# Performance work log

Hardware: AMD Instinct MI355X
Metric: run time of the kernel (lower is better)

The kernel has to match this reference:

```python
import jax, jax.numpy as jnp
import numpy as np

TOP_K = 8
NUM_EXPERTS = 256
HIDDEN = 7168
NUM_TOKENS = 16384
NORM_TOPK_PROB = True


def setup_inputs() -> dict:
    key = jax.random.key(0)
    k1, k2 = jax.random.split(key)
    hidden_states = jax.random.normal(k1, (NUM_TOKENS, HIDDEN), dtype=jnp.float32)
    weight = jax.random.normal(k2, (NUM_EXPERTS, HIDDEN), dtype=jnp.float32) * 0.02
    return {"hidden_states": hidden_states, "weight": weight}


def reference(hidden_states, weight):
    # Router logits: [T, E] = [T, H] @ [E, H]^T
    logits = jnp.einsum("th,eh->te", hidden_states, weight)
    # Fused softmax + top-k (npu_moe_gating_top_k_softmax semantics):
    # softmax over experts, then take top-k probabilities and their indices.
    probs = jax.nn.softmax(logits, axis=-1)
    topk_weight, topk_idx = jax.lax.top_k(probs, TOP_K)  # [T, k]
    # row_idx: expert-major (column-major) flattened row indices, as the NPU op returns.
    T = logits.shape[0]
    row_idx = jnp.arange(T * TOP_K, dtype=jnp.int32).reshape(TOP_K, T).T  # [T, k]
    if TOP_K > 1 and NORM_TOPK_PROB:
        denominator = jnp.sum(topk_weight, axis=-1, keepdims=True) + 1e-20
        topk_weight = topk_weight / denominator
    topk_idx = topk_idx.astype(jnp.int32)
    return (topk_idx, topk_weight, row_idx)
```

## Files before the change

### kernel.cpp

```cpp
#include <hip/hip_runtime.h>
#include <hip/hip_bf16.h>

#define NTOK 16384
#define HID 7168
#define NEXP 256
#define TOPK 8

#define BT 64
#define BK 64
#define NCH (HID / BK)

typedef __bf16 bf16x8 __attribute__((ext_vector_type(8)));
typedef float  f32x16 __attribute__((ext_vector_type(16)));

typedef __attribute__((address_space(1))) const unsigned char ga_t;
typedef __attribute__((address_space(3))) unsigned char la_t;

__device__ __align__(16) unsigned short g_wb[NEXP * HID];

__device__ __forceinline__ unsigned int f2bfb(float x) {
    unsigned int u = __float_as_uint(x);
    return (u + 0x7fffu + ((u >> 16) & 1u)) >> 16;
}

__device__ __forceinline__ void gll16(const void* g, void* l) {
    __builtin_amdgcn_global_load_lds((ga_t*)g, (la_t*)l, 16, 0, 0);
}

__device__ __forceinline__ bf16x8 cvt8(float4 p, float4 q) {
    union { bf16x8 v; __hip_bfloat162 h[4]; } c;
    c.h[0] = __float22bfloat162_rn(make_float2(p.x, p.y));
    c.h[1] = __float22bfloat162_rn(make_float2(p.z, p.w));
    c.h[2] = __float22bfloat162_rn(make_float2(q.x, q.y));
    c.h[3] = __float22bfloat162_rn(make_float2(q.z, q.w));
    return c.v;
}

__global__ void wconv(const float* __restrict__ wt) {
    const int i = blockIdx.x * 256 + threadIdx.x;
    const float4 v = ((const float4*)wt)[i];
    uint2 o;
    o.x = f2bfb(v.x) | (f2bfb(v.y) << 16);
    o.y = f2bfb(v.z) | (f2bfb(v.w) << 16);
    ((uint2*)g_wb)[i] = o;
}

__global__ void moe_rows(float* __restrict__ ob) {
    const int q = blockIdx.x * 256 + threadIdx.x;
    ob[262144 + q] = (float)((q & 7) * NTOK + (q >> 3));
}

__global__ __launch_bounds__(512) void moe_gate_v11(
    const float* __restrict__ hs,
    float* __restrict__ ob)
{
    __shared__ __align__(16) char smem[147456];

    const int tid  = threadIdx.x;
    const int t0   = blockIdx.x * BT;
    const int lane = tid & 63;
    const int wv   = tid >> 6;
    const int wm   = wv >> 2;
    const int wn   = wv & 3;

    const char* aS[2];
    int aD[2];
    #pragma unroll
    for (int i = 0; i < 2; ++i) {
        const int r = wv * 8 + i * 4 + (lane >> 4);
        const int cs = (((lane & 15) << 4) ^ ((r & 15) << 4));
        aS[i] = (const char*)hs + ((size_t)(t0 + r) * HID) * 4 + cs;
        aD[i] = (wv * 8 + i * 4) * 256;
    }
    const char* bS[4];
    int bD[4];
    #pragma unroll
    for (int i = 0; i < 4; ++i) {
        const int e = wv * 32 + i * 8 + (lane >> 3);
        const int cs = (((lane & 7) << 4) ^ (((lane >> 3) & 7) << 4));
        bS[i] = (const char*)g_wb + (size_t)e * HID * 2 + cs;
        bD[i] = 16384 + (wv * 32 + i * 8) * 128;
    }

    const int khalf = lane >> 5;
    const int rowA  = wm * 32 + (lane & 31);
    const int aswz  = (rowA & 15) << 4;
    const int rowB  = wn * 64 + (lane & 31);
    const int bswz  = (rowB & 7) << 4;

    f32x16 acc0 = {};
    f32x16 acc1 = {};

    auto ISSUE = [&](int s, char* p) {
        #pragma unroll
        for (int i = 0; i < 2; ++i)
            gll16(aS[i] + (size_t)s * 256, p + aD[i]);
        #pragma unroll
        for (int i = 0; i < 4; ++i)
            gll16(bS[i] + (size_t)s * 128, p + bD[i]);
    };

    auto COMPUTE = [&](const char* p) {
        const char* A  = p;
        const char* Bp = p + 16384;
        #pragma unroll
        for (int kk = 0; kk < 4; ++kk) {
            const int ca = kk * 64 + khalf * 32;
            float4 a0 = *(const float4*)(A + rowA * 256 + ((ca     ) ^ aswz));
            float4 a1 = *(const float4*)(A + rowA * 256 + ((ca + 16) ^ aswz));
            bf16x8 a  = cvt8(a0, a1);
            const int cb = (kk * 32 + khalf * 16) ^ bswz;
            bf16x8 b0 = *(const bf16x8*)(Bp + rowB * 128 + cb);
            bf16x8 b1 = *(const bf16x8*)(Bp + (rowB + 32) * 128 + cb);
            acc0 = __builtin_amdgcn_mfma_f32_32x32x16_bf16(a, b0, acc0, 0, 0, 0);
            acc1 = __builtin_amdgcn_mfma_f32_32x32x16_bf16(a, b1, acc1, 0, 0, 0);
        }
    };

    char* p0 = smem;
    char* p1 = smem + 49152;
    char* p2 = smem + 98304;

    ISSUE(0, p0);
    ISSUE(1, p1);

    for (int s = 0; s < NCH - 2; ++s) {
        ISSUE(s + 2, p2);
        asm volatile("s_waitcnt vmcnt(12)" ::: "memory");
        __builtin_amdgcn_s_barrier();
        __builtin_amdgcn_sched_barrier(0);
        COMPUTE(p0);
        __builtin_amdgcn_s_barrier();
        __builtin_amdgcn_sched_barrier(0);
        char* t = p0; p0 = p1; p1 = p2; p2 = t;
    }
    asm volatile("s_waitcnt vmcnt(6)" ::: "memory");
    __builtin_amdgcn_s_barrier();
    __builtin_amdgcn_sched_barrier(0);
    COMPUTE(p0);
    __builtin_amdgcn_s_barrier();
    __builtin_amdgcn_sched_barrier(0);
    { char* t = p0; p0 = p1; p1 = p2; p2 = t; }
    asm volatile("s_waitcnt vmcnt(0)" ::: "memory");
    __builtin_amdgcn_s_barrier();
    __builtin_amdgcn_sched_barrier(0);
    COMPUTE(p0);
    __syncthreads();

    float* ll = (float*)smem;
    {
        const int ec = wn * 64 + (lane & 31);
        const int rb = wm * 32 + 4 * (lane >> 5);
        #pragma unroll
        for (int r = 0; r < 16; ++r) {
            const int tok = rb + (r & 3) + 8 * (r >> 2);
            ll[tok * 257 + ec]      = acc0[r];
            ll[tok * 257 + ec + 32] = acc1[r];
        }
    }
    __syncthreads();

    if (tid < BT) {
        const float* lr = ll + tid * 257;
        float bv[TOPK]; int bi8[TOPK];
        #pragma unroll
        for (int k = 0; k < TOPK; ++k) { bv[k] = -1e30f; bi8[k] = 0; }
        for (int e = 0; e < NEXP; ++e) {
            const float v = lr[e];
            if (v > bv[TOPK - 1]) {
                int k = TOPK - 1;
                while (k > 0 && v > bv[k - 1]) {
                    bv[k] = bv[k - 1]; bi8[k] = bi8[k - 1]; --k;
                }
                bv[k] = v; bi8[k] = e;
            }
        }
        float ev[TOPK], ssum = 0.f;
        #pragma unroll
        for (int r = 0; r < TOPK; ++r) { ev[r] = expf(bv[r] - bv[0]); ssum += ev[r]; }
        const float inv = 1.0f / ssum;

        const int tg = t0 + tid;
        #pragma unroll
        for (int r = 0; r < TOPK; ++r) {
            ob[(size_t)tg * TOPK + r]          = (float)bi8[r];
            ob[131072 + (size_t)tg * TOPK + r] = ev[r] * inv;
        }
    }
}

extern "C" void kernel_launch(void* const* d_in, const int* in_sizes, int n_in,
                              void* d_out, int out_size, void* d_ws, size_t ws_size,
                              hipStream_t stream) {
    const float* hs = (const float*)d_in[0];
    const float* wt = (const float*)d_in[1];
    float* ob = (float*)d_out;

    wconv<<<dim3(NEXP * HID / 4 / 256), dim3(256), 0, stream>>>(wt);
    moe_gate_v11<<<dim3(NTOK / BT), dim3(512), 0, stream>>>(hs, ob);
    moe_rows<<<dim3(512), dim3(256), 0, stream>>>(ob);
}
```

Measured before the change: 296.2 us.

## Pre-layout bf16 weights in MFMA fragment order and load B directly to registers

The weight conversion kernel now writes the bf16 weights in MFMA B-fragment order. The GEMM kernel loads B straight from global memory into registers, double-buffered in two register arrays, instead of staging it through LDS. Only the fp32 hidden-state tiles stay in LDS, with a larger K step of 128 and double buffering, which cuts LDS from 144KB to about 65KB and may allow more blocks per CU. The trade-off is much higher register pressure from holding 32 uint4 B fragments per thread, plus B loads that depend on L2 hits without LDS reuse.

```diff
diff --git a/kernel.cpp b/kernel.cpp
--- a/kernel.cpp
+++ b/kernel.cpp
@@ -7,8 +7,8 @@
 #define TOPK 8
 
 #define BT 64
-#define BK 64
-#define NCH (HID / BK)
+#define BK 128
+#define NPH (HID / BK)
 
 typedef __bf16 bf16x8 __attribute__((ext_vector_type(8)));
 typedef float  f32x16 __attribute__((ext_vector_type(16)));
@@ -22,11 +22,20 @@
     unsigned int u = __float_as_uint(x);
     return (u + 0x7fffu + ((u >> 16) & 1u)) >> 16;
 }
-
+__device__ __forceinline__ uint4 pk4(float4 p, float4 q) {
+    uint4 u;
+    u.x = f2bfb(p.x) | (f2bfb(p.y) << 16);
+    u.y = f2bfb(p.z) | (f2bfb(p.w) << 16);
+    u.z = f2bfb(q.x) | (f2bfb(q.y) << 16);
+    u.w = f2bfb(q.z) | (f2bfb(q.w) << 16);
+    return u;
+}
+__device__ __forceinline__ bf16x8 asbf8(uint4 u) {
+    union { uint4 a; bf16x8 b; } c; c.a = u; return c.b;
+}
 __device__ __forceinline__ void gll16(const void* g, void* l) {
     __builtin_amdgcn_global_load_lds((ga_t*)g, (la_t*)l, 16, 0, 0);
 }
-
 __device__ __forceinline__ bf16x8 cvt8(float4 p, float4 q) {
     union { bf16x8 v; __hip_bfloat162 h[4]; } c;
     c.h[0] = __float22bfloat162_rn(make_float2(p.x, p.y));
@@ -36,13 +45,16 @@
     return c.v;
 }
 
-__global__ void wconv(const float* __restrict__ wt) {
-    const int i = blockIdx.x * 256 + threadIdx.x;
-    const float4 v = ((const float4*)wt)[i];
-    uint2 o;
-    o.x = f2bfb(v.x) | (f2bfb(v.y) << 16);
-    o.y = f2bfb(v.z) | (f2bfb(v.w) << 16);
-    ((uint2*)g_wb)[i] = o;
+__global__ void wconv_frag(const float* __restrict__ wt) {
+    const int tid = blockIdx.x * 256 + threadIdx.x;
+    const int l  = tid & 63;
+    const int ks = (tid >> 6) & 7;
+    const int g  = (tid >> 9) & 7;
+    const int p  = tid >> 12;
+    const int e  = g * 32 + (l & 31);
+    const int kb = p * 128 + ks * 16 + ((l >> 5) << 3);
+    const float4* s = (const float4*)(wt + (size_t)e * HID + kb);
+    ((uint4*)g_wb)[tid] = pk4(s[0], s[1]);
 }
 
 __global__ void moe_rows(float* __restrict__ ob) {
@@ -50,11 +62,13 @@
     ob[262144 + q] = (float)((q & 7) * NTOK + (q >> 3));
 }
 
-__global__ __launch_bounds__(512) void moe_gate_v11(
+__global__ __launch_bounds__(512) void moe_gate_v12(
     const float* __restrict__ hs,
     float* __restrict__ ob)
 {
-    __shared__ __align__(16) char smem[147456];
+    __shared__ __align__(16) char smem[66560];
+    char* const bufA0 = smem;
+    char* const bufA1 = smem + 32768;
 
     const int tid  = threadIdx.x;
     const int t0   = blockIdx.x * BT;
@@ -63,88 +77,98 @@
     const int wm   = wv >> 2;
     const int wn   = wv & 3;
 
-    const char* aS[2];
-    int aD[2];
-    #pragma unroll
-    for (int i = 0; i < 2; ++i) {
-        const int r = wv * 8 + i * 4 + (lane >> 4);
-        const int cs = (((lane & 15) << 4) ^ ((r & 15) << 4));
-        aS[i] = (const char*)hs + ((size_t)(t0 + r) * HID) * 4 + cs;
-        aD[i] = (wv * 8 + i * 4) * 256;
-    }
-    const char* bS[4];
-    int bD[4];
+    const char* aS[4];
+    int aD[4];
     #pragma unroll
     for (int i = 0; i < 4; ++i) {
-        const int e = wv * 32 + i * 8 + (lane >> 3);
-        const int cs = (((lane & 7) << 4) ^ (((lane >> 3) & 7) << 4));
-        bS[i] = (const char*)g_wb + (size_t)e * HID * 2 + cs;
-        bD[i] = 16384 + (wv * 32 + i * 8) * 128;
+        const int r2 = (wv * 4 + i) * 2 + (lane >> 5);
+        const int cs = ((lane & 31) * 16) ^ ((r2 & 31) << 4);
+        aS[i] = (const char*)hs + (size_t)(t0 + r2) * HID * 4 + cs;
+        aD[i] = (wv * 4 + i) * 1024;
     }
 
     const int khalf = lane >> 5;
     const int rowA  = wm * 32 + (lane & 31);
-    const int aswz  = (rowA & 15) << 4;
-    const int rowB  = wn * 64 + (lane & 31);
-    const int bswz  = (rowB & 7) << 4;
+    const int abase = rowA * 512;
+    const int aswz  = (rowA & 31) << 4;
+
+    const char* const wbB = (const char*)g_wb + (size_t)(wn * 2) * 8192 + lane * 16;
 
     f32x16 acc0 = {};
     f32x16 acc1 = {};
 
-    auto ISSUE = [&](int s, char* p) {
-        #pragma unroll
-        for (int i = 0; i < 2; ++i)
-            gll16(aS[i] + (size_t)s * 256, p + aD[i]);
-        #pragma unroll
-        for (int i = 0; i < 4; ++i)
-            gll16(bS[i] + (size_t)s * 128, p + bD[i]);
-    };
-
-    auto COMPUTE = [&](const char* p) {
-        const char* A  = p;
-        const char* Bp = p + 16384;
-        #pragma unroll
-        for (int kk = 0; kk < 4; ++kk) {
-            const int ca = kk * 64 + khalf * 32;
-            float4 a0 = *(const float4*)(A + rowA * 256 + ((ca     ) ^ aswz));
-            float4 a1 = *(const float4*)(A + rowA * 256 + ((ca + 16) ^ aswz));
-            bf16x8 a  = cvt8(a0, a1);
-            const int cb = (kk * 32 + khalf * 16) ^ bswz;
-            bf16x8 b0 = *(const bf16x8*)(Bp + rowB * 128 + cb);
-            bf16x8 b1 = *(const bf16x8*)(Bp + (rowB + 32) * 128 + cb);
-            acc0 = __builtin_amdgcn_mfma_f32_32x32x16_bf16(a, b0, acc0, 0, 0, 0);
-            acc1 = __builtin_amdgcn_mfma_f32_32x32x16_bf16(a, b1, acc1, 0, 0, 0);
-        }
-    };
-
-    char* p0 = smem;
-    char* p1 = smem + 49152;
-    char* p2 = smem + 98304;
-
-    ISSUE(0, p0);
-    ISSUE(1, p1);
-
-    for (int s = 0; s < NCH - 2; ++s) {
-        ISSUE(s + 2, p2);
-        asm volatile("s_waitcnt vmcnt(12)" ::: "memory");
-        __builtin_amdgcn_s_barrier();
-        __builtin_amdgcn_sched_barrier(0);
-        COMPUTE(p0);
-        __builtin_amdgcn_s_barrier();
-        __builtin_amdgcn_sched_barrier(0);
-        char* t = p0; p0 = p1; p1 = p2; p2 = t;
-    }
-    asm volatile("s_waitcnt vmcnt(6)" ::: "memory");
-    __builtin_amdgcn_s_barrier();
-    __builtin_amdgcn_sched_barrier(0);
-    COMPUTE(p0);
-    __builtin_amdgcn_s_barrier();
-    __builtin_amdgcn_sched_barrier(0);
-    { char* t = p0; p0 = p1; p1 = p2; p2 = t; }
-    asm volatile("s_waitcnt vmcnt(0)" ::: "memory");
-    __builtin_amdgcn_s_barrier();
-    __builtin_amdgcn_sched_barrier(0);
-    COMPUTE(p0);
+    uint4 s0[16];
+    uint4 s1[16];
+
+#define ISSUE_A(P, BUF)                                                       \
+    do {                                                                      \
+        _Pragma("unroll")                                                     \
+        for (int i = 0; i < 4; ++i)                                           \
+            gll16(aS[i] + (size_t)(P) * 512, (BUF) + aD[i]);                  \
+        __builtin_amdgcn_sched_barrier(0);                                    \
+    } while (0)
+
+#define ISSUE_B(P, ARR)                                                       \
+    do {                                                                      \
+        const char* bp = wbB + (size_t)(P) * 65536;                           \
+        _Pragma("unroll")                                                     \
+        for (int c = 0; c < 2; ++c)                                           \
+            _Pragma("unroll")                                                 \
+            for (int ks = 0; ks < 8; ++ks)                                    \
+                ARR[c * 8 + ks] = *(const uint4*)(bp + c * 8192 + ks * 1024); \
+        __builtin_amdgcn_sched_barrier(0);                                    \
+    } while (0)
+
+#define COMPUTE(BUF, ARR)                                                     \
+    do {                                                                      \
+        _Pragma("unroll")                                                     \
+        for (int ks = 0; ks < 8; ++ks) {                                      \
+            const int o = ks * 64 + khalf * 32;                               \
+            float4 a0 = *(const float4*)((BUF) + abase + ((o     ) ^ aswz));  \
+            float4 a1 = *(const float4*)((BUF) + abase + ((o + 16) ^ aswz));  \
+            bf16x8 a = cvt8(a0, a1);                                          \
+            acc0 = __builtin_amdgcn_mfma_f32_32x32x16_bf16(a, asbf8(ARR[ks]),     acc0, 0, 0, 0); \
+            acc1 = __builtin_amdgcn_mfma_f32_32x32x16_bf16(a, asbf8(ARR[8 + ks]), acc1, 0, 0, 0); \
+        }                                                                     \
+    } while (0)
+
+#define WAITBAR(VM)                                                           \
+    do {                                                                      \
+        asm volatile("s_waitcnt vmcnt(" #VM ")" ::: "memory");                \
+        __builtin_amdgcn_sched_barrier(0);                                    \
+        __builtin_amdgcn_s_barrier();                                         \
+        __builtin_amdgcn_sched_barrier(0);                                    \
+    } while (0)
+
+#define ENDBAR()                                                              \
+    do {                                                                      \
+        __builtin_amdgcn_s_barrier();                                         \
+        __builtin_amdgcn_sched_barrier(0);                                    \
+    } while (0)
+
+    ISSUE_B(0, s0);
+    ISSUE_A(0, bufA0);
+    ISSUE_A(1, bufA1);
+
+    for (int p = 0; p < 54; p += 2) {
+        ISSUE_B(p + 1, s1);
+        WAITBAR(20);
+        COMPUTE(bufA0, s0);
+        ENDBAR();
+        ISSUE_A(p + 2, bufA0);
+
+        ISSUE_B(p + 2, s0);
+        WAITBAR(20);
+        COMPUTE(bufA1, s1);
+        ENDBAR();
+        if (p + 3 < NPH) ISSUE_A(p + 3, bufA1);
+    }
+    ISSUE_B(55, s1);
+    WAITBAR(20);
+    COMPUTE(bufA0, s0);
+    ENDBAR();
+    WAITBAR(0);
+    COMPUTE(bufA1, s1);
     __syncthreads();
 
     float* ll = (float*)smem;
@@ -187,6 +211,11 @@
             ob[131072 + (size_t)tg * TOPK + r] = ev[r] * inv;
         }
     }
+#undef ISSUE_A
+#undef ISSUE_B
+#undef COMPUTE
+#undef WAITBAR
+#undef ENDBAR
 }
 
 extern "C" void kernel_launch(void* const* d_in, const int* in_sizes, int n_in,
@@ -196,7 +225,7 @@
     const float* wt = (const float*)d_in[1];
     float* ob = (float*)d_out;
 
-    wconv<<<dim3(NEXP * HID / 4 / 256), dim3(256), 0, stream>>>(wt);
-    moe_gate_v11<<<dim3(NTOK / BT), dim3(512), 0, stream>>>(hs, ob);
+    wconv_frag<<<dim3(NEXP * HID / 8 / 256), dim3(256), 0, stream>>>(wt);
+    moe_gate_v12<<<dim3(NTOK / BT), dim3(512), 0, stream>>>(hs, ob);
     moe_rows<<<dim3(512), dim3(256), 0, stream>>>(ob);
 }
```

Result: faster. 248.3 us (-16.2%).

## Split-K router GEMM with swizzled bf16 weights and separate reduce+top-k kernel

Applied to the files above, without the earlier changes.

Replaces the single 256-block GEMM+top-k kernel with a split-K GEMM (4 K-slices, 1024 blocks of 256 threads, smaller LDS so three blocks fit per CU) that writes partial logits to workspace. A new reduce kernel sums the partials and performs the top-k softmax. The weight conversion now pre-swizzles bf16 weights into a k-chunk-major layout so B tiles load contiguously. This raises parallelism and occupancy beyond the 256 blocks of the old grid, at the cost of writing and re-reading 4x16384x256 fp32 partials (about 64 MB) and an extra launch.

```diff
diff --git a/kernel.cpp b/kernel.cpp
--- a/kernel.cpp
+++ b/kernel.cpp
@@ -6,10 +6,6 @@
 #define NEXP 256
 #define TOPK 8
 
-#define BT 64
-#define BK 64
-#define NCH (HID / BK)
-
 typedef __bf16 bf16x8 __attribute__((ext_vector_type(8)));
 typedef float  f32x16 __attribute__((ext_vector_type(16)));
 
@@ -22,11 +18,17 @@
     unsigned int u = __float_as_uint(x);
     return (u + 0x7fffu + ((u >> 16) & 1u)) >> 16;
 }
-
+__device__ __forceinline__ uint4 pk4(float4 p, float4 q) {
+    uint4 u;
+    u.x = f2bfb(p.x) | (f2bfb(p.y) << 16);
+    u.y = f2bfb(p.z) | (f2bfb(p.w) << 16);
+    u.z = f2bfb(q.x) | (f2bfb(q.y) << 16);
+    u.w = f2bfb(q.z) | (f2bfb(q.w) << 16);
+    return u;
+}
 __device__ __forceinline__ void gll16(const void* g, void* l) {
     __builtin_amdgcn_global_load_lds((ga_t*)g, (la_t*)l, 16, 0, 0);
 }
-
 __device__ __forceinline__ bf16x8 cvt8(float4 p, float4 q) {
     union { bf16x8 v; __hip_bfloat162 h[4]; } c;
     c.h[0] = __float22bfloat162_rn(make_float2(p.x, p.y));
@@ -36,13 +38,14 @@
     return c.v;
 }
 
-__global__ void wconv(const float* __restrict__ wt) {
-    const int i = blockIdx.x * 256 + threadIdx.x;
-    const float4 v = ((const float4*)wt)[i];
-    uint2 o;
-    o.x = f2bfb(v.x) | (f2bfb(v.y) << 16);
-    o.y = f2bfb(v.z) | (f2bfb(v.w) << 16);
-    ((uint2*)g_wb)[i] = o;
+__global__ void wconv_swz(const float* __restrict__ wt) {
+    const int t   = blockIdx.x * 256 + threadIdx.x;
+    const int y16 = t & 1023;
+    const int kc  = t >> 10;
+    const int e   = y16 >> 2;
+    const int sl  = (y16 & 3) ^ (e & 3);
+    const float4* s = (const float4*)(wt + (size_t)e * HID + kc * 32 + sl * 8);
+    ((uint4*)g_wb)[t] = pk4(s[0], s[1]);
 }
 
 __global__ void moe_rows(float* __restrict__ ob) {
@@ -50,117 +53,129 @@
     ob[262144 + q] = (float)((q & 7) * NTOK + (q >> 3));
 }
 
-__global__ __launch_bounds__(512) void moe_gate_v11(
+template<int KS>
+__global__ __launch_bounds__(256, 3) void moe_gate_v14(
     const float* __restrict__ hs,
+    float* __restrict__ pw)
+{
+    constexpr int KLEN = HID / KS;
+    constexpr int NPH  = KLEN / 32;
+    __shared__ __align__(16) char smem[49152];
+
+    const int tid   = threadIdx.x;
+    const int lane  = tid & 63;
+    const int w     = tid >> 6;
+    const int tg    = w >> 1;
+    const int h     = w & 1;
+    const int t0    = blockIdx.x * 64;
+    const int by    = blockIdx.y;
+    const int khalf = lane >> 5;
+
+    const char* aS[2];
+    #pragma unroll
+    for (int ii = 0; ii < 2; ++ii) {
+        const int row  = (w * 2 + ii) * 8 + (lane >> 3);
+        const int aoff = (((lane & 7) ^ ((lane >> 3) & 7)) << 4);
+        aS[ii] = (const char*)hs + (size_t)(t0 + row) * (HID * 4)
+               + (size_t)by * (KLEN * 4) + aoff;
+    }
+    const char* bS = (const char*)g_wb + (size_t)by * NPH * 16384
+                   + (w * 4) * 1024 + lane * 16;
+
+    f32x16 acc0 = {}, acc1 = {}, acc2 = {}, acc3 = {};
+
+    auto ISSUE = [&](int p, int bi) {
+        char* bA = smem + bi * 8192;
+        char* bB = smem + 16384 + bi * 16384;
+        #pragma unroll
+        for (int ii = 0; ii < 2; ++ii)
+            gll16(aS[ii] + (size_t)p * 128, bA + (w * 2 + ii) * 1024);
+        #pragma unroll
+        for (int iv = 0; iv < 4; ++iv)
+            gll16(bS + (size_t)p * 16384 + iv * 1024, bB + (w * 4 + iv) * 1024);
+    };
+
+    const int rowA = tg * 32 + (lane & 31);
+    const int aswz = (rowA & 7) << 4;
+    const int e0   = h * 128 + (lane & 31);
+    const int bswz = (e0 & 3) << 4;
+
+    auto COMPUTE = [&](int bi) {
+        const char* bA = smem + bi * 8192;
+        const char* bB = smem + 16384 + bi * 16384;
+        #pragma unroll
+        for (int s = 0; s < 2; ++s) {
+            const int ca = s * 64 + khalf * 32;
+            float4 a0 = *(const float4*)(bA + rowA * 128 + ((ca     ) ^ aswz));
+            float4 a1 = *(const float4*)(bA + rowA * 128 + ((ca + 16) ^ aswz));
+            bf16x8 a = cvt8(a0, a1);
+            const int cb = (s * 32 + khalf * 16) ^ bswz;
+            bf16x8 b0 = *(const bf16x8*)(bB + (e0      ) * 64 + cb);
+            bf16x8 b1 = *(const bf16x8*)(bB + (e0 + 32 ) * 64 + cb);
+            bf16x8 b2 = *(const bf16x8*)(bB + (e0 + 64 ) * 64 + cb);
+            bf16x8 b3 = *(const bf16x8*)(bB + (e0 + 96 ) * 64 + cb);
+            acc0 = __builtin_amdgcn_mfma_f32_32x32x16_bf16(a, b0, acc0, 0, 0, 0);
+            acc1 = __builtin_amdgcn_mfma_f32_32x32x16_bf16(a, b1, acc1, 0, 0, 0);
+            acc2 = __builtin_amdgcn_mfma_f32_32x32x16_bf16(a, b2, acc2, 0, 0, 0);
+            acc3 = __builtin_amdgcn_mfma_f32_32x32x16_bf16(a, b3, acc3, 0, 0, 0);
+        }
+    };
+
+    ISSUE(0, 0);
+    for (int p = 0; p < NPH - 1; ++p) {
+        ISSUE(p + 1, (p + 1) & 1);
+        asm volatile("s_waitcnt vmcnt(6)" ::: "memory");
+        __builtin_amdgcn_sched_barrier(0);
+        __builtin_amdgcn_s_barrier();
+        __builtin_amdgcn_sched_barrier(0);
+        COMPUTE(p & 1);
+        __builtin_amdgcn_s_barrier();
+        __builtin_amdgcn_sched_barrier(0);
+    }
+    asm volatile("s_waitcnt vmcnt(0)" ::: "memory");
+    __builtin_amdgcn_sched_barrier(0);
+    __builtin_amdgcn_s_barrier();
+    __builtin_amdgcn_sched_barrier(0);
+    COMPUTE((NPH - 1) & 1);
+
+    float* base = pw + ((size_t)by * NTOK + t0) * 256;
+    #pragma unroll
+    for (int r = 0; r < 16; ++r) {
+        const int tok = tg * 32 + (r & 3) + 8 * (r >> 2) + 4 * khalf;
+        float* rp = base + (size_t)tok * 256 + h * 128 + (lane & 31);
+        rp[0]  = acc0[r];
+        rp[32] = acc1[r];
+        rp[64] = acc2[r];
+        rp[96] = acc3[r];
+    }
+}
+
+template<int KS>
+__global__ __launch_bounds__(256) void moe_reduce(
+    const float* __restrict__ pw,
     float* __restrict__ ob)
 {
-    __shared__ __align__(16) char smem[147456];
-
-    const int tid  = threadIdx.x;
-    const int t0   = blockIdx.x * BT;
-    const int lane = tid & 63;
-    const int wv   = tid >> 6;
-    const int wm   = wv >> 2;
-    const int wn   = wv & 3;
-
-    const char* aS[2];
-    int aD[2];
+    __shared__ float ll[64 * 257];
+    const int tid = threadIdx.x;
+    const size_t ro = (size_t)blockIdx.x * 16384;
+    const size_t PS = (size_t)NTOK * 256;
+
     #pragma unroll
-    for (int i = 0; i < 2; ++i) {
-        const int r = wv * 8 + i * 4 + (lane >> 4);
-        const int cs = (((lane & 15) << 4) ^ ((r & 15) << 4));
-        aS[i] = (const char*)hs + ((size_t)(t0 + r) * HID) * 4 + cs;
-        aD[i] = (wv * 8 + i * 4) * 256;
-    }
-    const char* bS[4];
-    int bD[4];
-    #pragma unroll
-    for (int i = 0; i < 4; ++i) {
-        const int e = wv * 32 + i * 8 + (lane >> 3);
-        const int cs = (((lane & 7) << 4) ^ (((lane >> 3) & 7) << 4));
-        bS[i] = (const char*)g_wb + (size_t)e * HID * 2 + cs;
-        bD[i] = 16384 + (wv * 32 + i * 8) * 128;
-    }
-
-    const int khalf = lane >> 5;
-    const int rowA  = wm * 32 + (lane & 31);
-    const int aswz  = (rowA & 15) << 4;
-    const int rowB  = wn * 64 + (lane & 31);
-    const int bswz  = (rowB & 7) << 4;
-
-    f32x16 acc0 = {};
-    f32x16 acc1 = {};
-
-    auto ISSUE = [&](int s, char* p) {
-        #pragma unroll
-        for (int i = 0; i < 2; ++i)
-            gll16(aS[i] + (size_t)s * 256, p + aD[i]);
-        #pragma unroll
-        for (int i = 0; i < 4; ++i)
-            gll16(bS[i] + (size_t)s * 128, p + bD[i]);
-    };
-
-    auto COMPUTE = [&](const char* p) {
-        const char* A  = p;
-        const char* Bp = p + 16384;
-        #pragma unroll
-        for (int kk = 0; kk < 4; ++kk) {
-            const int ca = kk * 64 + khalf * 32;
-            float4 a0 = *(const float4*)(A + rowA * 256 + ((ca     ) ^ aswz));
-            float4 a1 = *(const float4*)(A + rowA * 256 + ((ca + 16) ^ aswz));
-            bf16x8 a  = cvt8(a0, a1);
-            const int cb = (kk * 32 + khalf * 16) ^ bswz;
-            bf16x8 b0 = *(const bf16x8*)(Bp + rowB * 128 + cb);
-            bf16x8 b1 = *(const bf16x8*)(Bp + (rowB + 32) * 128 + cb);
-            acc0 = __builtin_amdgcn_mfma_f32_32x32x16_bf16(a, b0, acc0, 0, 0, 0);
-            acc1 = __builtin_amdgcn_mfma_f32_32x32x16_bf16(a, b1, acc1, 0, 0, 0);
-        }
-    };
-
-    char* p0 = smem;
-    char* p1 = smem + 49152;
-    char* p2 = smem + 98304;
-
-    ISSUE(0, p0);
-    ISSUE(1, p1);
-
-    for (int s = 0; s < NCH - 2; ++s) {
-        ISSUE(s + 2, p2);
-        asm volatile("s_waitcnt vmcnt(12)" ::: "memory");
-        __builtin_amdgcn_s_barrier();
-        __builtin_amdgcn_sched_barrier(0);
-        COMPUTE(p0);
-        __builtin_amdgcn_s_barrier();
-        __builtin_amdgcn_sched_barrier(0);
-        char* t = p0; p0 = p1; p1 = p2; p2 = t;
-    }
-    asm volatile("s_waitcnt vmcnt(6)" ::: "memory");
-    __builtin_amdgcn_s_barrier();
-    __builtin_amdgcn_sched_barrier(0);
-    COMPUTE(p0);
-    __builtin_amdgcn_s_barrier();
-    __builtin_amdgcn_sched_barrier(0);
-    { char* t = p0; p0 = p1; p1 = p2; p2 = t; }
-    asm volatile("s_waitcnt vmcnt(0)" ::: "memory");
-    __builtin_amdgcn_s_barrier();
-    __builtin_amdgcn_sched_barrier(0);
-    COMPUTE(p0);
+    for (int j = 0; j < 16; ++j) {
+        const size_t f = (size_t)j * 1024 + tid * 4;
+        float4 v = *(const float4*)(pw + ro + f);
+        #pragma unroll
+        for (int s = 1; s < KS; ++s) {
+            float4 u = *(const float4*)(pw + s * PS + ro + f);
+            v.x += u.x; v.y += u.y; v.z += u.z; v.w += u.w;
+        }
+        const int t = (int)(f >> 8);
+        const int e = (int)(f & 255);
+        *(float4*)&ll[t * 257 + e] = v;
+    }
     __syncthreads();
 
-    float* ll = (float*)smem;
-    {
-        const int ec = wn * 64 + (lane & 31);
-        const int rb = wm * 32 + 4 * (lane >> 5);
-        #pragma unroll
-        for (int r = 0; r < 16; ++r) {
-            const int tok = rb + (r & 3) + 8 * (r >> 2);
-            ll[tok * 257 + ec]      = acc0[r];
-            ll[tok * 257 + ec + 32] = acc1[r];
-        }
-    }
-    __syncthreads();
-
-    if (tid < BT) {
+    if (tid < 64) {
         const float* lr = ll + tid * 257;
         float bv[TOPK]; int bi8[TOPK];
         #pragma unroll
@@ -180,7 +195,7 @@
         for (int r = 0; r < TOPK; ++r) { ev[r] = expf(bv[r] - bv[0]); ssum += ev[r]; }
         const float inv = 1.0f / ssum;
 
-        const int tg = t0 + tid;
+        const int tg = blockIdx.x * 64 + tid;
         #pragma unroll
         for (int r = 0; r < TOPK; ++r) {
             ob[(size_t)tg * TOPK + r]          = (float)bi8[r];
@@ -195,8 +210,17 @@
     const float* hs = (const float*)d_in[0];
     const float* wt = (const float*)d_in[1];
     float* ob = (float*)d_out;
-
-    wconv<<<dim3(NEXP * HID / 4 / 256), dim3(256), 0, stream>>>(wt);
-    moe_gate_v11<<<dim3(NTOK / BT), dim3(512), 0, stream>>>(hs, ob);
+    float* pw = (float*)d_ws;
+
+    wconv_swz<<<dim3(NEXP * HID * 2 / 16 / 256), dim3(256), 0, stream>>>(wt);
+
+    const size_t need4 = (size_t)4 * NTOK * NEXP * sizeof(float);
+    if (ws_size >= need4) {
+        moe_gate_v14<4><<<dim3(256, 4), dim3(256), 0, stream>>>(hs, pw);
+        moe_reduce<4><<<dim3(256), dim3(256), 0, stream>>>(pw, ob);
+    } else {
+        moe_gate_v14<1><<<dim3(256, 1), dim3(256), 0, stream>>>(hs, pw);
+        moe_reduce<1><<<dim3(256), dim3(256), 0, stream>>>(pw, ob);
+    }
     moe_rows<<<dim3(512), dim3(256), 0, stream>>>(ob);
 }
```

After: 269.6 us. 1.1x faster.
